# Kernel optimization log

Measured on AMD Instinct MI355X. Metric: run time of the kernel, lower is better.

The kernel has to match this reference:

```python
import jax, jax.numpy as jnp
import numpy as np

EMBED = 1024
HEAD = 64
CTX = 2048


def setup_inputs() -> dict:
    key = jax.random.key(0)
    ks = jax.random.split(key, 7)
    scale = 1.0 / np.sqrt(EMBED)
    return {
        "x": jax.random.normal(ks[0], (8, CTX, EMBED), dtype=jnp.float32),
        "Wq": jax.random.normal(ks[1], (EMBED, HEAD), dtype=jnp.float32) * scale,
        "bq": jax.random.normal(ks[2], (HEAD,), dtype=jnp.float32) * 0.01,
        "Wk": jax.random.normal(ks[3], (EMBED, HEAD), dtype=jnp.float32) * scale,
        "bk": jax.random.normal(ks[4], (HEAD,), dtype=jnp.float32) * 0.01,
        "Wv": jax.random.normal(ks[5], (EMBED, HEAD), dtype=jnp.float32) * scale,
        "bv": jax.random.normal(ks[6], (HEAD,), dtype=jnp.float32) * 0.01,
    }


def reference(x, Wq, bq, Wk, bk, Wv, bv):
    # x: [B, T, E]
    q = x @ Wq + bq  # [B, T, H]
    k = x @ Wk + bk
    v = x @ Wv + bv
    scores = jnp.einsum("bqh,bkh->bqk", q, k) / jnp.sqrt(jnp.float32(HEAD))
    T = x.shape[1]
    causal = jnp.tril(jnp.ones((T, T), dtype=bool))
    scores = jnp.where(causal, scores, -jnp.inf)
    attn = jax.nn.softmax(scores, axis=-1)  # dropout=0.0 -> identity
    out = jnp.einsum("bqk,bkh->bqh", attn, v)
    return out
```

## Files before the change

### kernel.cpp

```cpp
#include <hip/hip_runtime.h>
#include <math.h>
#include <stdint.h>

#define BDIM 8
#define TDIM 2048
#define EDIM 1024
#define HDIM 64
#define NCHUNK 80

typedef short bf16x8 __attribute__((ext_vector_type(8)));
typedef float f32x4 __attribute__((ext_vector_type(4)));
typedef uint32_t u32x2 __attribute__((ext_vector_type(2)));

__device__ __forceinline__ unsigned short f2bf(float f) {
    uint32_t u = __builtin_bit_cast(uint32_t, f);
    u += 0x7fffu + ((u >> 16) & 1u);
    return (unsigned short)(u >> 16);
}
__device__ __forceinline__ float bf2f(unsigned short s) {
    uint32_t u = ((uint32_t)s) << 16;
    return __builtin_bit_cast(float, u);
}
__device__ __forceinline__ uint32_t cvt_pk_bf16(float lo, float hi) {
    uint32_t r;
    asm("v_cvt_pk_bf16_f32 %0, %1, %2" : "=v"(r) : "v"(lo), "v"(hi));
    return r;
}

__global__ __launch_bounds__(256) void prep_w(
    const float* __restrict__ Wq, const float* __restrict__ Wk,
    const float* __restrict__ Wv,
    unsigned short* __restrict__ WqT, unsigned short* __restrict__ WkT,
    unsigned short* __restrict__ WvT)
{
    int id = blockIdx.x * 256 + threadIdx.x;
    int e = id >> 6, h = id & 63;
    int oi = h * EDIM + e;
    WqT[oi] = f2bf(Wq[id]);
    WkT[oi] = f2bf(Wk[id]);
    WvT[oi] = f2bf(Wv[id]);
}

__global__ __launch_bounds__(256) void proj_kernel(
    const float* __restrict__ x,
    const unsigned short* __restrict__ WqT, const unsigned short* __restrict__ WkT,
    const unsigned short* __restrict__ WvT,
    const float* __restrict__ bq, const float* __restrict__ bk,
    const float* __restrict__ bv,
    unsigned short* __restrict__ Qb, unsigned short* __restrict__ Kb,
    unsigned short* __restrict__ VbT)
{
    __shared__ unsigned short Xs[2][64][72];
    __shared__ unsigned short Wqs[2][64][72];
    __shared__ unsigned short Wks[2][64][72];
    __shared__ unsigned short Wvs[2][64][72];

    const int t = threadIdx.x;
    const int lane = t & 63, w = t >> 6, quad = lane >> 4, ln = lane & 15;
    const int row0 = blockIdx.x * 64;
    const int sr = t >> 2;
    const int sc = (t & 3) << 4;

    f32x4 accq[4], acck[4], accv[4];
#pragma unroll
    for (int j = 0; j < 4; ++j) {
        accq[j] = (f32x4)(0.f); acck[j] = (f32x4)(0.f); accv[j] = (f32x4)(0.f);
    }

    const float* xp0  = &x[(size_t)(row0 + sr) * EDIM + sc];
    const size_t wrow = (size_t)sr * EDIM + sc;

    {
        float4 x0 = *(const float4*)(xp0);
        float4 x1 = *(const float4*)(xp0 + 4);
        float4 x2 = *(const float4*)(xp0 + 8);
        float4 x3 = *(const float4*)(xp0 + 12);
        bf16x8 xb0, xb1;
        xb0[0]=(short)f2bf(x0.x); xb0[1]=(short)f2bf(x0.y); xb0[2]=(short)f2bf(x0.z); xb0[3]=(short)f2bf(x0.w);
        xb0[4]=(short)f2bf(x1.x); xb0[5]=(short)f2bf(x1.y); xb0[6]=(short)f2bf(x1.z); xb0[7]=(short)f2bf(x1.w);
        xb1[0]=(short)f2bf(x2.x); xb1[1]=(short)f2bf(x2.y); xb1[2]=(short)f2bf(x2.z); xb1[3]=(short)f2bf(x2.w);
        xb1[4]=(short)f2bf(x3.x); xb1[5]=(short)f2bf(x3.y); xb1[6]=(short)f2bf(x3.z); xb1[7]=(short)f2bf(x3.w);
        *(bf16x8*)&Xs[0][sr][sc]     = xb0;
        *(bf16x8*)&Xs[0][sr][sc + 8] = xb1;
        *(bf16x8*)&Wqs[0][sr][sc]     = *(const bf16x8*)&WqT[wrow];
        *(bf16x8*)&Wqs[0][sr][sc + 8] = *(const bf16x8*)&WqT[wrow + 8];
        *(bf16x8*)&Wks[0][sr][sc]     = *(const bf16x8*)&WkT[wrow];
        *(bf16x8*)&Wks[0][sr][sc + 8] = *(const bf16x8*)&WkT[wrow + 8];
        *(bf16x8*)&Wvs[0][sr][sc]     = *(const bf16x8*)&WvT[wrow];
        *(bf16x8*)&Wvs[0][sr][sc + 8] = *(const bf16x8*)&WvT[wrow + 8];
    }

    for (int kt = 0; kt < EDIM / 64; ++kt) {
        const int cur = kt & 1, nxt = cur ^ 1;

        float4 x0, x1, x2, x3;
        bf16x8 wq0, wq1, wk0, wk1, wv0, wv1;
        if (kt < 15) {
            const float* xp = xp0 + (kt + 1) * 64;
            x0 = *(const float4*)(xp);
            x1 = *(const float4*)(xp + 4);
            x2 = *(const float4*)(xp + 8);
            x3 = *(const float4*)(xp + 12);
            const size_t wo = wrow + (kt + 1) * 64;
            wq0 = *(const bf16x8*)&WqT[wo];
            wq1 = *(const bf16x8*)&WqT[wo + 8];
            wk0 = *(const bf16x8*)&WkT[wo];
            wk1 = *(const bf16x8*)&WkT[wo + 8];
            wv0 = *(const bf16x8*)&WvT[wo];
            wv1 = *(const bf16x8*)&WvT[wo + 8];
        }

        __syncthreads();

        bf16x8 xa0 = *(const bf16x8*)&Xs[cur][16 * w + ln][8 * quad];
        bf16x8 xa1 = *(const bf16x8*)&Xs[cur][16 * w + ln][32 + 8 * quad];
#pragma unroll
        for (int j = 0; j < 4; ++j) {
            bf16x8 w0, w1;
            w0 = *(const bf16x8*)&Wqs[cur][16 * j + ln][8 * quad];
            w1 = *(const bf16x8*)&Wqs[cur][16 * j + ln][32 + 8 * quad];
            accq[j] = __builtin_amdgcn_mfma_f32_16x16x32_bf16(xa0, w0, accq[j], 0, 0, 0);
            accq[j] = __builtin_amdgcn_mfma_f32_16x16x32_bf16(xa1, w1, accq[j], 0, 0, 0);
            w0 = *(const bf16x8*)&Wks[cur][16 * j + ln][8 * quad];
            w1 = *(const bf16x8*)&Wks[cur][16 * j + ln][32 + 8 * quad];
            acck[j] = __builtin_amdgcn_mfma_f32_16x16x32_bf16(xa0, w0, acck[j], 0, 0, 0);
            acck[j] = __builtin_amdgcn_mfma_f32_16x16x32_bf16(xa1, w1, acck[j], 0, 0, 0);
            w0 = *(const bf16x8*)&Wvs[cur][16 * j + ln][8 * quad];
            w1 = *(const bf16x8*)&Wvs[cur][16 * j + ln][32 + 8 * quad];
            accv[j] = __builtin_amdgcn_mfma_f32_16x16x32_bf16(xa0, w0, accv[j], 0, 0, 0);
            accv[j] = __builtin_amdgcn_mfma_f32_16x16x32_bf16(xa1, w1, accv[j], 0, 0, 0);
        }

        if (kt < 15) {
            bf16x8 xb0, xb1;
            xb0[0]=(short)f2bf(x0.x); xb0[1]=(short)f2bf(x0.y); xb0[2]=(short)f2bf(x0.z); xb0[3]=(short)f2bf(x0.w);
            xb0[4]=(short)f2bf(x1.x); xb0[5]=(short)f2bf(x1.y); xb0[6]=(short)f2bf(x1.z); xb0[7]=(short)f2bf(x1.w);
            xb1[0]=(short)f2bf(x2.x); xb1[1]=(short)f2bf(x2.y); xb1[2]=(short)f2bf(x2.z); xb1[3]=(short)f2bf(x2.w);
            xb1[4]=(short)f2bf(x3.x); xb1[5]=(short)f2bf(x3.y); xb1[6]=(short)f2bf(x3.z); xb1[7]=(short)f2bf(x3.w);
            *(bf16x8*)&Xs[nxt][sr][sc]     = xb0;
            *(bf16x8*)&Xs[nxt][sr][sc + 8] = xb1;
            *(bf16x8*)&Wqs[nxt][sr][sc]     = wq0;
            *(bf16x8*)&Wqs[nxt][sr][sc + 8] = wq1;
            *(bf16x8*)&Wks[nxt][sr][sc]     = wk0;
            *(bf16x8*)&Wks[nxt][sr][sc + 8] = wk1;
            *(bf16x8*)&Wvs[nxt][sr][sc]     = wv0;
            *(bf16x8*)&Wvs[nxt][sr][sc + 8] = wv1;
        }
    }

#pragma unroll
    for (int j = 0; j < 4; ++j) {
        int col = 16 * j + ln;
        float bqv = bq[col], bkv = bk[col], bvv = bv[col];
#pragma unroll
        for (int r = 0; r < 4; ++r) {
            size_t row = (size_t)(row0 + 16 * w + 4 * quad + r);
            Qb[row * HDIM + col] = f2bf(accq[j][r] + bqv);
            Kb[row * HDIM + col] = f2bf(acck[j][r] + bkv);
            int bb = (int)(row >> 11);
            int tr = (int)(row & 2047);
            VbT[((size_t)bb * HDIM + col) * TDIM + tr] = f2bf(accv[j][r] + bvv);
        }
    }
}

__global__ __launch_bounds__(256) void attn_partial(
    const unsigned short* __restrict__ Qb, const unsigned short* __restrict__ Kb,
    const unsigned short* __restrict__ VbT,
    unsigned short* __restrict__ PO, float* __restrict__ Pm, float* __restrict__ Pl)
{
    __shared__ unsigned short Ks[2][64][72];
    __shared__ unsigned short VsT[2][64][72];
    __shared__ unsigned short Ps[64][72];

    const int t = threadIdx.x;
    const int lane = t & 63, w = t >> 6, quad = lane >> 4, ln = lane & 15;
    const int f = blockIdx.x;
    const int b = blockIdx.y;

    int g = 0;
    while (f >= 4 * (g + 1) * (g + 2)) ++g;
    const int r_  = f - 4 * g * (g + 1);
    const int iq  = 8 * g + r_ / (g + 1);
    const int ch  = r_ % (g + 1);

    const int q0 = iq * 64;
    const size_t base = (size_t)b * TDIM * HDIM;
    const int sr = t >> 2;
    const int sc = (t & 3) << 4;

    const size_t qrow = base + (size_t)(q0 + 16 * w + ln) * HDIM;
    bf16x8 qa0 = *(const bf16x8*)&Qb[qrow + 8 * quad];
    bf16x8 qa1 = *(const bf16x8*)&Qb[qrow + 32 + 8 * quad];

    f32x4 od[4];
#pragma unroll
    for (int j = 0; j < 4; ++j) od[j] = (f32x4)(0.f);
    float m_run = -INFINITY, l_run = 0.f;

    const float scale = 0.125f;
    const int jt0 = 8 * ch;
    int j1 = jt0 + 7; if (j1 > iq) j1 = iq;

    {
        size_t ko = base + (size_t)(jt0 * 64 + sr) * HDIM + sc;
        *(bf16x8*)&Ks[0][sr][sc]     = *(const bf16x8*)&Kb[ko];
        *(bf16x8*)&Ks[0][sr][sc + 8] = *(const bf16x8*)&Kb[ko + 8];
        const unsigned short* vrow =
            &VbT[((size_t)b * HDIM + sr) * TDIM + jt0 * 64 + sc];
        *(bf16x8*)&VsT[0][sr][sc]     = *(const bf16x8*)vrow;
        *(bf16x8*)&VsT[0][sr][sc + 8] = *(const bf16x8*)(vrow + 8);
    }

    for (int jt = jt0; jt <= j1; ++jt) {
        const int cur = (jt - jt0) & 1, nxt = cur ^ 1;

        bf16x8 kn0, kn1, vn0, vn1;
        if (jt < j1) {
            size_t ko = base + (size_t)((jt + 1) * 64 + sr) * HDIM + sc;
            kn0 = *(const bf16x8*)&Kb[ko];
            kn1 = *(const bf16x8*)&Kb[ko + 8];
            const unsigned short* vrow =
                &VbT[((size_t)b * HDIM + sr) * TDIM + (jt + 1) * 64 + sc];
            vn0 = *(const bf16x8*)vrow;
            vn1 = *(const bf16x8*)(vrow + 8);
        }

        __syncthreads();

        f32x4 s[4];
        __builtin_amdgcn_s_setprio(1);
#pragma unroll
        for (int j = 0; j < 4; ++j) {
            bf16x8 kb0 = *(const bf16x8*)&Ks[cur][16 * j + ln][8 * quad];
            bf16x8 kb1 = *(const bf16x8*)&Ks[cur][16 * j + ln][32 + 8 * quad];
            s[j] = (f32x4)(0.f);
            s[j] = __builtin_amdgcn_mfma_f32_16x16x32_bf16(kb0, qa0, s[j], 0, 0, 0);
            s[j] = __builtin_amdgcn_mfma_f32_16x16x32_bf16(kb1, qa1, s[j], 0, 0, 0);
        }
        __builtin_amdgcn_s_setprio(0);

        const int qg = q0 + 16 * w + ln;
        if (jt == iq) {
#pragma unroll
            for (int j = 0; j < 4; ++j) {
#pragma unroll
                for (int r = 0; r < 4; ++r) {
                    int kg = jt * 64 + 16 * j + 4 * quad + r;
                    s[j][r] = (kg <= qg) ? s[j][r] * scale : -INFINITY;
                }
            }
        } else {
#pragma unroll
            for (int j = 0; j < 4; ++j)
#pragma unroll
                for (int r = 0; r < 4; ++r) s[j][r] *= scale;
        }

        float mx;
        {
            float a0 = fmaxf(fmaxf(s[0][0], s[0][1]), fmaxf(s[0][2], s[0][3]));
            float a1 = fmaxf(fmaxf(s[1][0], s[1][1]), fmaxf(s[1][2], s[1][3]));
            float a2 = fmaxf(fmaxf(s[2][0], s[2][1]), fmaxf(s[2][2], s[2][3]));
            float a3 = fmaxf(fmaxf(s[3][0], s[3][1]), fmaxf(s[3][2], s[3][3]));
            mx = fmaxf(fmaxf(a0, a1), fmaxf(a2, a3));
        }
        mx = fmaxf(mx, __shfl_xor(mx, 16));
        mx = fmaxf(mx, __shfl_xor(mx, 32));

        float mn = fmaxf(m_run, mx);
        float al = __expf(m_run - mn);
        m_run = mn;

        float rs = 0.f;
#pragma unroll
        for (int j = 0; j < 4; ++j) {
            float p0 = __expf(s[j][0] - mn);
            float p1 = __expf(s[j][1] - mn);
            float p2 = __expf(s[j][2] - mn);
            float p3 = __expf(s[j][3] - mn);
            s[j][0] = p0; s[j][1] = p1; s[j][2] = p2; s[j][3] = p3;
            rs += (p0 + p1) + (p2 + p3);
        }
        rs += __shfl_xor(rs, 16);
        rs += __shfl_xor(rs, 32);
        l_run = l_run * al + rs;

#pragma unroll
        for (int j = 0; j < 4; ++j) {
            u32x2 pk;
            pk.x = cvt_pk_bf16(s[j][0], s[j][1]);
            pk.y = cvt_pk_bf16(s[j][2], s[j][3]);
            *(u32x2*)&Ps[16 * w + ln][16 * j + 4 * quad] = pk;
        }

#pragma unroll
        for (int r = 0; r < 4; ++r) {
            float alr = __shfl(al, 4 * quad + r);
#pragma unroll
            for (int j = 0; j < 4; ++j) od[j][r] *= alr;
        }

        bf16x8 pa0 = *(const bf16x8*)&Ps[16 * w + ln][8 * quad];
        bf16x8 pa1 = *(const bf16x8*)&Ps[16 * w + ln][32 + 8 * quad];
        __builtin_amdgcn_s_setprio(1);
#pragma unroll
        for (int j = 0; j < 4; ++j) {
            bf16x8 vb0 = *(const bf16x8*)&VsT[cur][16 * j + ln][8 * quad];
            bf16x8 vb1 = *(const bf16x8*)&VsT[cur][16 * j + ln][32 + 8 * quad];
            od[j] = __builtin_amdgcn_mfma_f32_16x16x32_bf16(pa0, vb0, od[j], 0, 0, 0);
            od[j] = __builtin_amdgcn_mfma_f32_16x16x32_bf16(pa1, vb1, od[j], 0, 0, 0);
        }
        __builtin_amdgcn_s_setprio(0);

        if (jt < j1) {
            *(bf16x8*)&Ks[nxt][sr][sc]     = kn0;
            *(bf16x8*)&Ks[nxt][sr][sc + 8] = kn1;
            *(bf16x8*)&VsT[nxt][sr][sc]     = vn0;
            *(bf16x8*)&VsT[nxt][sr][sc + 8] = vn1;
        }
    }

    const size_t p = (size_t)b * NCHUNK + f;
#pragma unroll
    for (int j = 0; j < 4; ++j)
#pragma unroll
        for (int r = 0; r < 4; ++r)
            PO[p * 4096 + (size_t)(16 * w + 4 * quad + r) * 64 + 16 * j + ln] =
                f2bf(od[j][r]);
    if (quad == 0) {
        Pm[p * 64 + 16 * w + ln] = m_run;
        Pl[p * 64 + 16 * w + ln] = l_run;
    }
}

__global__ __launch_bounds__(256) void attn_combine(
    const unsigned short* __restrict__ PO, const float* __restrict__ Pm,
    const float* __restrict__ Pl, float* __restrict__ out)
{
    const int iq = blockIdx.x, b = blockIdx.y;
    const int g = iq >> 3;
    const int nch = g + 1;
    const int fbase = 4 * g * (g + 1) + (iq - 8 * g) * (g + 1);
    const int t = threadIdx.x;
    const int row = t >> 2;
    const int c0 = (t & 3) << 4;
    const size_t pbase = (size_t)b * NCHUNK + fbase;

    float M = -INFINITY;
    for (int c = 0; c < nch; ++c)
        M = fmaxf(M, Pm[(pbase + c) * 64 + row]);

    float a[16];
#pragma unroll
    for (int i = 0; i < 16; ++i) a[i] = 0.f;
    float L = 0.f;
    for (int c = 0; c < nch; ++c) {
        size_t p = pbase + c;
        float sc = __expf(Pm[p * 64 + row] - M);
        L += sc * Pl[p * 64 + row];
        const unsigned short* po = &PO[p * 4096 + (size_t)row * 64 + c0];
        bf16x8 v0 = *(const bf16x8*)(po);
        bf16x8 v1 = *(const bf16x8*)(po + 8);
#pragma unroll
        for (int i = 0; i < 8; ++i) {
            a[i]     += sc * bf2f((unsigned short)v0[i]);
            a[8 + i] += sc * bf2f((unsigned short)v1[i]);
        }
    }
    float li = 1.f / L;
    float4 o0, o1, o2, o3;
    o0.x=a[0]*li;  o0.y=a[1]*li;  o0.z=a[2]*li;  o0.w=a[3]*li;
    o1.x=a[4]*li;  o1.y=a[5]*li;  o1.z=a[6]*li;  o1.w=a[7]*li;
    o2.x=a[8]*li;  o2.y=a[9]*li;  o2.z=a[10]*li; o2.w=a[11]*li;
    o3.x=a[12]*li; o3.y=a[13]*li; o3.z=a[14]*li; o3.w=a[15]*li;
    float* op = &out[((size_t)b * TDIM + (size_t)iq * 64 + row) * HDIM + c0];
    *(float4*)(op)      = o0;
    *(float4*)(op + 4)  = o1;
    *(float4*)(op + 8)  = o2;
    *(float4*)(op + 12) = o3;
}

extern "C" void kernel_launch(void* const* d_in, const int* in_sizes, int n_in,
                              void* d_out, int out_size, void* d_ws, size_t ws_size,
                              hipStream_t stream) {
    const float* x  = (const float*)d_in[0];
    const float* Wq = (const float*)d_in[1];
    const float* bq = (const float*)d_in[2];
    const float* Wk = (const float*)d_in[3];
    const float* bk = (const float*)d_in[4];
    const float* Wv = (const float*)d_in[5];
    const float* bv = (const float*)d_in[6];
    float* out = (float*)d_out;

    const size_t n = (size_t)BDIM * TDIM * HDIM;
    unsigned short* Qb  = (unsigned short*)d_ws;
    unsigned short* Kb  = Qb + n;
    unsigned short* VbT = Kb + n;
    unsigned short* WqT = VbT + n;
    unsigned short* WkT = WqT + (size_t)EDIM * HDIM;
    unsigned short* WvT = WkT + (size_t)EDIM * HDIM;
    unsigned short* PO  = WvT + (size_t)EDIM * HDIM;
    float* Pm = (float*)(PO + (size_t)BDIM * NCHUNK * 4096);
    float* Pl = Pm + (size_t)BDIM * NCHUNK * 64;

    prep_w<<<dim3(EDIM * HDIM / 256), 256, 0, stream>>>(Wq, Wk, Wv, WqT, WkT, WvT);
    proj_kernel<<<dim3(BDIM * TDIM / 64), 256, 0, stream>>>(
        x, WqT, WkT, WvT, bq, bk, bv, Qb, Kb, VbT);
    attn_partial<<<dim3(NCHUNK, BDIM), 256, 0, stream>>>(Qb, Kb, VbT, PO, Pm, Pl);
    attn_combine<<<dim3(TDIM / 64, BDIM), 256, 0, stream>>>(PO, Pm, Pl, out);
}
```

Baseline: 143.0 us.

## Fuse combine into attention via last-block atomic counter and shrink projection tiles

```diff
diff --git a/kernel.cpp b/kernel.cpp
--- a/kernel.cpp
+++ b/kernel.cpp
@@ -31,7 +31,7 @@
     const float* __restrict__ Wq, const float* __restrict__ Wk,
     const float* __restrict__ Wv,
     unsigned short* __restrict__ WqT, unsigned short* __restrict__ WkT,
-    unsigned short* __restrict__ WvT)
+    unsigned short* __restrict__ WvT, int* __restrict__ cnt)
 {
     int id = blockIdx.x * 256 + threadIdx.x;
     int e = id >> 6, h = id & 63;
@@ -39,6 +39,7 @@
     WqT[oi] = f2bf(Wq[id]);
     WkT[oi] = f2bf(Wk[id]);
     WvT[oi] = f2bf(Wv[id]);
+    if (blockIdx.x == 0 && threadIdx.x < BDIM * 32) cnt[threadIdx.x] = 0;
 }
 
 __global__ __launch_bounds__(256) void proj_kernel(
@@ -50,38 +51,37 @@
     unsigned short* __restrict__ Qb, unsigned short* __restrict__ Kb,
     unsigned short* __restrict__ VbT)
 {
-    __shared__ unsigned short Xs[2][64][72];
+    __shared__ unsigned short Xs[2][32][72];
     __shared__ unsigned short Wqs[2][64][72];
     __shared__ unsigned short Wks[2][64][72];
     __shared__ unsigned short Wvs[2][64][72];
 
     const int t = threadIdx.x;
     const int lane = t & 63, w = t >> 6, quad = lane >> 4, ln = lane & 15;
-    const int row0 = blockIdx.x * 64;
+    const int row0 = blockIdx.x * 32;
+    const int wr = (w & 1) << 4;
+    const int jb = (w >> 1) << 1;
+    const int sxr = t >> 3;
+    const int sxc = (t & 7) << 3;
     const int sr = t >> 2;
     const int sc = (t & 3) << 4;
 
-    f32x4 accq[4], acck[4], accv[4];
-#pragma unroll
-    for (int j = 0; j < 4; ++j) {
+    f32x4 accq[2], acck[2], accv[2];
+#pragma unroll
+    for (int j = 0; j < 2; ++j) {
         accq[j] = (f32x4)(0.f); acck[j] = (f32x4)(0.f); accv[j] = (f32x4)(0.f);
     }
 
-    const float* xp0  = &x[(size_t)(row0 + sr) * EDIM + sc];
+    const float* xp0  = &x[(size_t)(row0 + sxr) * EDIM + sxc];
     const size_t wrow = (size_t)sr * EDIM + sc;
 
     {
         float4 x0 = *(const float4*)(xp0);
         float4 x1 = *(const float4*)(xp0 + 4);
-        float4 x2 = *(const float4*)(xp0 + 8);
-        float4 x3 = *(const float4*)(xp0 + 12);
-        bf16x8 xb0, xb1;
-        xb0[0]=(short)f2bf(x0.x); xb0[1]=(short)f2bf(x0.y); xb0[2]=(short)f2bf(x0.z); xb0[3]=(short)f2bf(x0.w);
-        xb0[4]=(short)f2bf(x1.x); xb0[5]=(short)f2bf(x1.y); xb0[6]=(short)f2bf(x1.z); xb0[7]=(short)f2bf(x1.w);
-        xb1[0]=(short)f2bf(x2.x); xb1[1]=(short)f2bf(x2.y); xb1[2]=(short)f2bf(x2.z); xb1[3]=(short)f2bf(x2.w);
-        xb1[4]=(short)f2bf(x3.x); xb1[5]=(short)f2bf(x3.y); xb1[6]=(short)f2bf(x3.z); xb1[7]=(short)f2bf(x3.w);
-        *(bf16x8*)&Xs[0][sr][sc]     = xb0;
-        *(bf16x8*)&Xs[0][sr][sc + 8] = xb1;
+        bf16x8 xb;
+        xb[0]=(short)f2bf(x0.x); xb[1]=(short)f2bf(x0.y); xb[2]=(short)f2bf(x0.z); xb[3]=(short)f2bf(x0.w);
+        xb[4]=(short)f2bf(x1.x); xb[5]=(short)f2bf(x1.y); xb[6]=(short)f2bf(x1.z); xb[7]=(short)f2bf(x1.w);
+        *(bf16x8*)&Xs[0][sxr][sxc] = xb;
         *(bf16x8*)&Wqs[0][sr][sc]     = *(const bf16x8*)&WqT[wrow];
         *(bf16x8*)&Wqs[0][sr][sc + 8] = *(const bf16x8*)&WqT[wrow + 8];
         *(bf16x8*)&Wks[0][sr][sc]     = *(const bf16x8*)&WkT[wrow];
@@ -93,14 +93,12 @@
     for (int kt = 0; kt < EDIM / 64; ++kt) {
         const int cur = kt & 1, nxt = cur ^ 1;
 
-        float4 x0, x1, x2, x3;
+        float4 x0, x1;
         bf16x8 wq0, wq1, wk0, wk1, wv0, wv1;
         if (kt < 15) {
             const float* xp = xp0 + (kt + 1) * 64;
             x0 = *(const float4*)(xp);
             x1 = *(const float4*)(xp + 4);
-            x2 = *(const float4*)(xp + 8);
-            x3 = *(const float4*)(xp + 12);
             const size_t wo = wrow + (kt + 1) * 64;
             wq0 = *(const bf16x8*)&WqT[wo];
             wq1 = *(const bf16x8*)&WqT[wo + 8];
@@ -112,33 +110,33 @@
 
         __syncthreads();
 
-        bf16x8 xa0 = *(const bf16x8*)&Xs[cur][16 * w + ln][8 * quad];
-        bf16x8 xa1 = *(const bf16x8*)&Xs[cur][16 * w + ln][32 + 8 * quad];
-#pragma unroll
-        for (int j = 0; j < 4; ++j) {
+        bf16x8 xa0 = *(const bf16x8*)&Xs[cur][wr + ln][8 * quad];
+        bf16x8 xa1 = *(const bf16x8*)&Xs[cur][wr + ln][32 + 8 * quad];
+        __builtin_amdgcn_s_setprio(1);
+#pragma unroll
+        for (int jj = 0; jj < 2; ++jj) {
+            const int j = jb + jj;
             bf16x8 w0, w1;
             w0 = *(const bf16x8*)&Wqs[cur][16 * j + ln][8 * quad];
             w1 = *(const bf16x8*)&Wqs[cur][16 * j + ln][32 + 8 * quad];
-            accq[j] = __builtin_amdgcn_mfma_f32_16x16x32_bf16(xa0, w0, accq[j], 0, 0, 0);
-            accq[j] = __builtin_amdgcn_mfma_f32_16x16x32_bf16(xa1, w1, accq[j], 0, 0, 0);
+            accq[jj] = __builtin_amdgcn_mfma_f32_16x16x32_bf16(xa0, w0, accq[jj], 0, 0, 0);
+            accq[jj] = __builtin_amdgcn_mfma_f32_16x16x32_bf16(xa1, w1, accq[jj], 0, 0, 0);
             w0 = *(const bf16x8*)&Wks[cur][16 * j + ln][8 * quad];
             w1 = *(const bf16x8*)&Wks[cur][16 * j + ln][32 + 8 * quad];
-            acck[j] = __builtin_amdgcn_mfma_f32_16x16x32_bf16(xa0, w0, acck[j], 0, 0, 0);
-            acck[j] = __builtin_amdgcn_mfma_f32_16x16x32_bf16(xa1, w1, acck[j], 0, 0, 0);
+            acck[jj] = __builtin_amdgcn_mfma_f32_16x16x32_bf16(xa0, w0, acck[jj], 0, 0, 0);
+            acck[jj] = __builtin_amdgcn_mfma_f32_16x16x32_bf16(xa1, w1, acck[jj], 0, 0, 0);
             w0 = *(const bf16x8*)&Wvs[cur][16 * j + ln][8 * quad];
             w1 = *(const bf16x8*)&Wvs[cur][16 * j + ln][32 + 8 * quad];
-            accv[j] = __builtin_amdgcn_mfma_f32_16x16x32_bf16(xa0, w0, accv[j], 0, 0, 0);
-            accv[j] = __builtin_amdgcn_mfma_f32_16x16x32_bf16(xa1, w1, accv[j], 0, 0, 0);
-        }
+            accv[jj] = __builtin_amdgcn_mfma_f32_16x16x32_bf16(xa0, w0, accv[jj], 0, 0, 0);
+            accv[jj] = __builtin_amdgcn_mfma_f32_16x16x32_bf16(xa1, w1, accv[jj], 0, 0, 0);
+        }
+        __builtin_amdgcn_s_setprio(0);
 
         if (kt < 15) {
-            bf16x8 xb0, xb1;
-            xb0[0]=(short)f2bf(x0.x); xb0[1]=(short)f2bf(x0.y); xb0[2]=(short)f2bf(x0.z); xb0[3]=(short)f2bf(x0.w);
-            xb0[4]=(short)f2bf(x1.x); xb0[5]=(short)f2bf(x1.y); xb0[6]=(short)f2bf(x1.z); xb0[7]=(short)f2bf(x1.w);
-            xb1[0]=(short)f2bf(x2.x); xb1[1]=(short)f2bf(x2.y); xb1[2]=(short)f2bf(x2.z); xb1[3]=(short)f2bf(x2.w);
-            xb1[4]=(short)f2bf(x3.x); xb1[5]=(short)f2bf(x3.y); xb1[6]=(short)f2bf(x3.z); xb1[7]=(short)f2bf(x3.w);
-            *(bf16x8*)&Xs[nxt][sr][sc]     = xb0;
-            *(bf16x8*)&Xs[nxt][sr][sc + 8] = xb1;
+            bf16x8 xb;
+            xb[0]=(short)f2bf(x0.x); xb[1]=(short)f2bf(x0.y); xb[2]=(short)f2bf(x0.z); xb[3]=(short)f2bf(x0.w);
+            xb[4]=(short)f2bf(x1.x); xb[5]=(short)f2bf(x1.y); xb[6]=(short)f2bf(x1.z); xb[7]=(short)f2bf(x1.w);
+            *(bf16x8*)&Xs[nxt][sxr][sxc] = xb;
             *(bf16x8*)&Wqs[nxt][sr][sc]     = wq0;
             *(bf16x8*)&Wqs[nxt][sr][sc + 8] = wq1;
             *(bf16x8*)&Wks[nxt][sr][sc]     = wk0;
@@ -149,29 +147,31 @@
     }
 
 #pragma unroll
-    for (int j = 0; j < 4; ++j) {
-        int col = 16 * j + ln;
+    for (int jj = 0; jj < 2; ++jj) {
+        int col = 16 * (jb + jj) + ln;
         float bqv = bq[col], bkv = bk[col], bvv = bv[col];
 #pragma unroll
         for (int r = 0; r < 4; ++r) {
-            size_t row = (size_t)(row0 + 16 * w + 4 * quad + r);
-            Qb[row * HDIM + col] = f2bf(accq[j][r] + bqv);
-            Kb[row * HDIM + col] = f2bf(acck[j][r] + bkv);
+            size_t row = (size_t)(row0 + wr + 4 * quad + r);
+            Qb[row * HDIM + col] = f2bf(accq[jj][r] + bqv);
+            Kb[row * HDIM + col] = f2bf(acck[jj][r] + bkv);
             int bb = (int)(row >> 11);
             int tr = (int)(row & 2047);
-            VbT[((size_t)bb * HDIM + col) * TDIM + tr] = f2bf(accv[j][r] + bvv);
-        }
-    }
-}
-
-__global__ __launch_bounds__(256) void attn_partial(
+            VbT[((size_t)bb * HDIM + col) * TDIM + tr] = f2bf(accv[jj][r] + bvv);
+        }
+    }
+}
+
+__global__ __launch_bounds__(256, 4) void attn_partial(
     const unsigned short* __restrict__ Qb, const unsigned short* __restrict__ Kb,
     const unsigned short* __restrict__ VbT,
-    unsigned short* __restrict__ PO, float* __restrict__ Pm, float* __restrict__ Pl)
+    unsigned short* __restrict__ PO, float* __restrict__ Pm, float* __restrict__ Pl,
+    float* __restrict__ out, int* __restrict__ cnt)
 {
     __shared__ unsigned short Ks[2][64][72];
     __shared__ unsigned short VsT[2][64][72];
     __shared__ unsigned short Ps[64][72];
+    __shared__ int sflag;
 
     const int t = threadIdx.x;
     const int lane = t & 63, w = t >> 6, quad = lane >> 4, ln = lane & 15;
@@ -183,6 +183,7 @@
     const int r_  = f - 4 * g * (g + 1);
     const int iq  = 8 * g + r_ / (g + 1);
     const int ch  = r_ % (g + 1);
+    const int nch = g + 1;
 
     const int q0 = iq * 64;
     const size_t base = (size_t)b * TDIM * HDIM;
@@ -321,6 +322,19 @@
         }
     }
 
+    if (nch == 1) {
+        float li[4];
+#pragma unroll
+        for (int r = 0; r < 4; ++r) li[r] = 1.f / __shfl(l_run, 4 * quad + r);
+#pragma unroll
+        for (int j = 0; j < 4; ++j)
+#pragma unroll
+            for (int r = 0; r < 4; ++r)
+                out[((size_t)b * TDIM + q0 + 16 * w + 4 * quad + r) * HDIM
+                    + 16 * j + ln] = od[j][r] * li[r];
+        return;
+    }
+
     const size_t p = (size_t)b * NCHUNK + f;
 #pragma unroll
     for (int j = 0; j < 4; ++j)
@@ -332,53 +346,55 @@
         Pm[p * 64 + 16 * w + ln] = m_run;
         Pl[p * 64 + 16 * w + ln] = l_run;
     }
-}
-
-__global__ __launch_bounds__(256) void attn_combine(
-    const unsigned short* __restrict__ PO, const float* __restrict__ Pm,
-    const float* __restrict__ Pl, float* __restrict__ out)
-{
-    const int iq = blockIdx.x, b = blockIdx.y;
-    const int g = iq >> 3;
-    const int nch = g + 1;
-    const int fbase = 4 * g * (g + 1) + (iq - 8 * g) * (g + 1);
-    const int t = threadIdx.x;
-    const int row = t >> 2;
-    const int c0 = (t & 3) << 4;
-    const size_t pbase = (size_t)b * NCHUNK + fbase;
-
-    float M = -INFINITY;
-    for (int c = 0; c < nch; ++c)
-        M = fmaxf(M, Pm[(pbase + c) * 64 + row]);
-
-    float a[16];
-#pragma unroll
-    for (int i = 0; i < 16; ++i) a[i] = 0.f;
-    float L = 0.f;
-    for (int c = 0; c < nch; ++c) {
-        size_t p = pbase + c;
-        float sc = __expf(Pm[p * 64 + row] - M);
-        L += sc * Pl[p * 64 + row];
-        const unsigned short* po = &PO[p * 4096 + (size_t)row * 64 + c0];
-        bf16x8 v0 = *(const bf16x8*)(po);
-        bf16x8 v1 = *(const bf16x8*)(po + 8);
-#pragma unroll
-        for (int i = 0; i < 8; ++i) {
-            a[i]     += sc * bf2f((unsigned short)v0[i]);
-            a[8 + i] += sc * bf2f((unsigned short)v1[i]);
-        }
-    }
-    float li = 1.f / L;
-    float4 o0, o1, o2, o3;
-    o0.x=a[0]*li;  o0.y=a[1]*li;  o0.z=a[2]*li;  o0.w=a[3]*li;
-    o1.x=a[4]*li;  o1.y=a[5]*li;  o1.z=a[6]*li;  o1.w=a[7]*li;
-    o2.x=a[8]*li;  o2.y=a[9]*li;  o2.z=a[10]*li; o2.w=a[11]*li;
-    o3.x=a[12]*li; o3.y=a[13]*li; o3.z=a[14]*li; o3.w=a[15]*li;
-    float* op = &out[((size_t)b * TDIM + (size_t)iq * 64 + row) * HDIM + c0];
-    *(float4*)(op)      = o0;
-    *(float4*)(op + 4)  = o1;
-    *(float4*)(op + 8)  = o2;
-    *(float4*)(op + 12) = o3;
+
+    __threadfence();
+    __syncthreads();
+    if (t == 0) {
+        int old = atomicAdd(&cnt[b * 32 + iq], 1);
+        sflag = (old == nch - 1);
+    }
+    __syncthreads();
+    if (!sflag) return;
+
+    __threadfence();
+    {
+        const int row = t >> 2;
+        const int c0 = (t & 3) << 4;
+        const size_t pbase = (size_t)b * NCHUNK + (size_t)(f - ch);
+
+        float M = -INFINITY;
+        for (int c = 0; c < nch; ++c)
+            M = fmaxf(M, Pm[(pbase + c) * 64 + row]);
+
+        float a[16];
+#pragma unroll
+        for (int i = 0; i < 16; ++i) a[i] = 0.f;
+        float L = 0.f;
+        for (int c = 0; c < nch; ++c) {
+            size_t pp = pbase + c;
+            float sc_ = __expf(Pm[pp * 64 + row] - M);
+            L += sc_ * Pl[pp * 64 + row];
+            const unsigned short* po = &PO[pp * 4096 + (size_t)row * 64 + c0];
+            bf16x8 v0 = *(const bf16x8*)(po);
+            bf16x8 v1 = *(const bf16x8*)(po + 8);
+#pragma unroll
+            for (int i = 0; i < 8; ++i) {
+                a[i]     += sc_ * bf2f((unsigned short)v0[i]);
+                a[8 + i] += sc_ * bf2f((unsigned short)v1[i]);
+            }
+        }
+        float li = 1.f / L;
+        float4 o0, o1, o2, o3;
+        o0.x=a[0]*li;  o0.y=a[1]*li;  o0.z=a[2]*li;  o0.w=a[3]*li;
+        o1.x=a[4]*li;  o1.y=a[5]*li;  o1.z=a[6]*li;  o1.w=a[7]*li;
+        o2.x=a[8]*li;  o2.y=a[9]*li;  o2.z=a[10]*li; o2.w=a[11]*li;
+        o3.x=a[12]*li; o3.y=a[13]*li; o3.z=a[14]*li; o3.w=a[15]*li;
+        float* op = &out[((size_t)b * TDIM + (size_t)iq * 64 + row) * HDIM + c0];
+        *(float4*)(op)      = o0;
+        *(float4*)(op + 4)  = o1;
+        *(float4*)(op + 8)  = o2;
+        *(float4*)(op + 12) = o3;
+    }
 }
 
 extern "C" void kernel_launch(void* const* d_in, const int* in_sizes, int n_in,
@@ -403,10 +419,11 @@
     unsigned short* PO  = WvT + (size_t)EDIM * HDIM;
     float* Pm = (float*)(PO + (size_t)BDIM * NCHUNK * 4096);
     float* Pl = Pm + (size_t)BDIM * NCHUNK * 64;
-
-    prep_w<<<dim3(EDIM * HDIM / 256), 256, 0, stream>>>(Wq, Wk, Wv, WqT, WkT, WvT);
-    proj_kernel<<<dim3(BDIM * TDIM / 64), 256, 0, stream>>>(
+    int*   cnt = (int*)(Pl + (size_t)BDIM * NCHUNK * 64);
+
+    prep_w<<<dim3(EDIM * HDIM / 256), 256, 0, stream>>>(Wq, Wk, Wv, WqT, WkT, WvT, cnt);
+    proj_kernel<<<dim3(BDIM * TDIM / 32), 256, 0, stream>>>(
         x, WqT, WkT, WvT, bq, bk, bv, Qb, Kb, VbT);
-    attn_partial<<<dim3(NCHUNK, BDIM), 256, 0, stream>>>(Qb, Kb, VbT, PO, Pm, Pl);
-    attn_combine<<<dim3(TDIM / 64, BDIM), 256, 0, stream>>>(PO, Pm, Pl, out);
-}
+    attn_partial<<<dim3(NCHUNK, BDIM), 256, 0, stream>>>(
+        Qb, Kb, VbT, PO, Pm, Pl, out, cnt);
+}
```

After: 243.2 us. 1.7x slower.
